# Performance work log

Measured on AMD Instinct MI355X. Metric: run time of the kernel, lower is better.

The kernel has to match this reference:

```python
import jax, jax.numpy as jnp
import numpy as np

B, NQ, S, D = 8, 1024, 2048, 512

def setup_inputs() -> dict:
    key = jax.random.key(0)
    k1, k2, k3, k4 = jax.random.split(key, 4)
    queries = jax.random.normal(k1, (B, NQ, D), dtype=jnp.float32)
    keys = jax.random.normal(k2, (B, S, D), dtype=jnp.float32)
    values = jax.random.normal(k3, (B, S, D), dtype=jnp.float32)
    mask = jax.random.randint(k4, (B, NQ, S), 0, 2, dtype=jnp.int32)
    return {"queries": queries, "keys": keys, "values": values, "mask": mask}

def reference(queries, keys, values, mask):
    # scores: dot-product attention scores (b, nq, s)
    scores = jnp.einsum('bqd,bsd->bqs', queries, keys)
    attention_dist = jax.nn.softmax(scores, axis=2)
    # mask then renormalize over seq axis
    attention_dist = attention_dist * mask.astype(attention_dist.dtype)
    attention_dist = attention_dist / attention_dist.sum(axis=2, keepdims=True)
    # weighted sum of values: equivalent to (dist.unsqueeze(3) * values.unsqueeze(1)).sum(2)
    final_vector = jnp.einsum('bqs,bsd->bqd', attention_dist, values)
    return final_vector
```

## Files before the change

kernel.cpp:

```cpp
#include <hip/hip_runtime.h>


#define Bz 8
#define NQz 1024
#define Sz 2048
#define Dz 512
#define QT 32
#define TS 32
#define NT ((Sz / 2) / TS)
#define KP 520
#define PP 40

typedef _Float16 f16x8 __attribute__((ext_vector_type(8)));
typedef float f32x4 __attribute__((ext_vector_type(4)));
typedef unsigned short ushort_t;

#define AS1(p) ((const __attribute__((address_space(1))) unsigned int*)(p))
#define AS3(p) ((__attribute__((address_space(3))) unsigned int*)(p))
#define DRAIN_ALL() __builtin_amdgcn_s_waitcnt(0)

__device__ __forceinline__ ushort_t f2h(float x) {
  _Float16 h = (_Float16)x;
  return __builtin_bit_cast(ushort_t, h);
}
__device__ __forceinline__ float h2f(ushort_t u) {
  return (float)__builtin_bit_cast(_Float16, u);
}

__global__ __launch_bounds__(256)
void prep(const float* __restrict__ K, const float* __restrict__ V,
          ushort_t* __restrict__ Kf, ushort_t* __restrict__ Vt) {
  __shared__ ushort_t sT[32][72];
  const int t = threadIdx.x;
  int bx = blockIdx.x;
  if (bx < 8192) {
    size_t e = ((size_t)bx * 256 + t) * 4;
    float4 v = *(const float4*)(K + e);
    uint2 w;
    w.x = (unsigned)f2h(v.x) | ((unsigned)f2h(v.y) << 16);
    w.y = (unsigned)f2h(v.z) | ((unsigned)f2h(v.w) << 16);
    *(uint2*)(Kf + e) = w;
    return;
  }
  bx -= 8192;
  const int b = bx >> 9;
  const int rest = bx & 511;
  const int st = rest >> 3;
  const int dt = rest & 7;
  const int s0 = st * 32, d0 = dt * 64;
  const float* Vb = V + ((size_t)b * Sz + s0) * Dz + d0;
#pragma unroll
  for (int i = 0; i < 2; ++i) {
    int idx = t + 256 * i;
    int s = idx >> 4;
    int dc = (idx & 15) * 4;
    float4 v = *(const float4*)(Vb + (size_t)s * Dz + dc);
    uint2 w;
    w.x = (unsigned)f2h(v.x) | ((unsigned)f2h(v.y) << 16);
    w.y = (unsigned)f2h(v.z) | ((unsigned)f2h(v.w) << 16);
    *(uint2*)(&sT[s][dc]) = w;
  }
  __syncthreads();
  ushort_t* VtB = Vt + ((size_t)b * Dz + d0) * Sz + s0;
  {
    int d = t >> 2, c = t & 3;
    uint4 u;
    ushort_t* tp = (ushort_t*)&u;
#pragma unroll
    for (int j = 0; j < 8; ++j) tp[j] = sT[c * 8 + j][d];
    *(uint4*)(VtB + (size_t)d * Sz + c * 8) = u;
  }
}

__global__ __launch_bounds__(256, 2)
void attn_flash(const float* __restrict__ Q, const int* __restrict__ Msk,
                const ushort_t* __restrict__ Kf, const ushort_t* __restrict__ Vt,
                float* __restrict__ Opart, float* __restrict__ Mpart,
                float* __restrict__ Lpart) {
  __shared__ ushort_t sK[TS][KP];
  __shared__ ushort_t sV[Dz][TS];
  __shared__ ushort_t sP[QT][PP];
  __shared__ float sTMax[2][QT];
  __shared__ float sTSum[2][QT];
  __shared__ float sM[2][QT];
  __shared__ float sL[2][QT];

  const int tid  = threadIdx.x;
  const int wave = tid >> 6;
  const int lane = tid & 63;
  const int l16  = lane & 15;
  const int quad = lane >> 4;
  const int rw   = wave & 1;
  const int cw   = wave >> 1;

  const int bx = blockIdx.x;
  const int b  = bx >> 6;
  const int r6 = bx & 63;
  const int qt = r6 >> 1;
  const int sh = r6 & 1;
  const int q0 = qt * QT;
  const int sbeg = sh * (Sz / 2);

  const float*    Qb  = Q  + ((size_t)b * NQz + q0) * Dz;
  const ushort_t* KfB = Kf + (size_t)b * Sz * Dz;
  const ushort_t* VtB = Vt + (size_t)b * Dz * Sz;
  const int*      Mb  = Msk + ((size_t)b * NQz + q0) * (size_t)Sz;

  int msk_r[4];

  auto issue_k = [&](int s0n) {
#pragma unroll
    for (int j = 0; j < 8; ++j) {
      int row = wave * 8 + j;
      const ushort_t* gp = KfB + (size_t)(s0n + row) * Dz + lane * 8;
      __builtin_amdgcn_global_load_lds(AS1(gp), AS3(&sK[row][0]), 16, 0, 0);
    }
  };
  auto issue_v = [&](int s0n) {
#pragma unroll
    for (int j = 0; j < 8; ++j) {
      int dbase = wave * 128 + j * 16;
      const ushort_t* gp =
          VtB + (size_t)(dbase + (lane >> 2)) * Sz + s0n + (lane & 3) * 8;
      __builtin_amdgcn_global_load_lds(AS1(gp), AS3(&sV[dbase][0]), 16, 0, 0);
    }
  };
  auto load_mask = [&](int s0n) {
    const int4 mv = *(const int4*)(Mb + (size_t)(rw * 16 + l16) * Sz + s0n +
                                   cw * 16 + quad * 4);
    msk_r[0] = mv.x; msk_r[1] = mv.y; msk_r[2] = mv.z; msk_r[3] = mv.w;
  };

  issue_k(sbeg);
  load_mask(sbeg);

  f16x8 qa[16];
  {
    const float* qrow = Qb + (size_t)(rw * 16 + l16) * Dz;
#pragma unroll
    for (int kk = 0; kk < 16; ++kk) {
      const float4 a = *(const float4*)(qrow + kk * 32 + quad * 8);
      const float4 c = *(const float4*)(qrow + kk * 32 + quad * 8 + 4);
      f16x8 h;
      h[0] = (_Float16)a.x; h[1] = (_Float16)a.y;
      h[2] = (_Float16)a.z; h[3] = (_Float16)a.w;
      h[4] = (_Float16)c.x; h[5] = (_Float16)c.y;
      h[6] = (_Float16)c.z; h[7] = (_Float16)c.w;
      qa[kk] = h;
    }
  }

  if (tid < QT) { sM[0][tid] = -1e30f; sL[0][tid] = 0.0f; }

  f32x4 oacc[16];
#pragma unroll
  for (int t = 0; t < 16; ++t) oacc[t] = (f32x4){0.f, 0.f, 0.f, 0.f};

  int p = 0;
  for (int i = 0; i < NT; ++i) {
    const int s0 = sbeg + i * TS;
    const int sNext = (i + 1 < NT) ? s0 + TS : sbeg;

    DRAIN_ALL();
    __syncthreads();

    issue_v(s0);

    f32x4 sc0 = (f32x4){0.f, 0.f, 0.f, 0.f};
    f32x4 sc1 = (f32x4){0.f, 0.f, 0.f, 0.f};
    {
      const ushort_t* kh = &sK[cw * 16 + l16][quad * 8];
#pragma unroll
      for (int kk = 0; kk < 16; kk += 2) {
        f16x8 b0 = *(const f16x8*)(kh + kk * 32);
        f16x8 b1 = *(const f16x8*)(kh + kk * 32 + 32);
        sc0 = __builtin_amdgcn_mfma_f32_16x16x32_f16(b0, qa[kk], sc0, 0, 0, 0);
        sc1 = __builtin_amdgcn_mfma_f32_16x16x32_f16(b1, qa[kk + 1], sc1, 0, 0, 0);
      }
    }
    f32x4 sc;
#pragma unroll
    for (int r = 0; r < 4; ++r) sc[r] = sc0[r] + sc1[r];

    float se[4];
#pragma unroll
    for (int r = 0; r < 4; ++r) se[r] = msk_r[r] ? sc[r] : -1e30f;
    float rmax = fmaxf(fmaxf(se[0], se[1]), fmaxf(se[2], se[3]));
    rmax = fmaxf(rmax, __shfl_xor(rmax, 16));
    rmax = fmaxf(rmax, __shfl_xor(rmax, 32));
    ushort_t pb[4];
    float rsum = 0.f;
#pragma unroll
    for (int r = 0; r < 4; ++r) {
      float pv = msk_r[r] ? __expf(se[r] - rmax) : 0.0f;
      pb[r] = f2h(pv);
      rsum += h2f(pb[r]);
    }
    {
      uint2 w;
      w.x = (unsigned)pb[0] | ((unsigned)pb[1] << 16);
      w.y = (unsigned)pb[2] | ((unsigned)pb[3] << 16);
      *(uint2*)(&sP[rw * 16 + l16][cw * 16 + quad * 4]) = w;
    }
    rsum += __shfl_xor(rsum, 16);
    rsum += __shfl_xor(rsum, 32);
    if (quad == 0) {
      sTMax[cw][rw * 16 + l16] = rmax;
      sTSum[cw][rw * 16 + l16] = rsum;
    }

    DRAIN_ALL();
    __syncthreads();

    issue_k(sNext);
    load_mask(sNext);

    const int pr = p;
    {
      const int row16 = rw * 16 + l16;
      float t0v = sTMax[0][row16], t1v = sTMax[1][row16];
      float mo16 = sM[pr][row16];
      float mn16 = fmaxf(mo16, fmaxf(t0v, t1v));
      float scl = __expf(((quad >> 1) ? t1v : t0v) - mn16);
      f16x8 praw = *(const f16x8*)(&sP[row16][quad * 8]);
      f16x8 pa;
#pragma unroll
      for (int j = 0; j < 8; ++j) pa[j] = (_Float16)((float)praw[j] * scl);

      float alpha[4];
#pragma unroll
      for (int r = 0; r < 4; ++r) {
        int rc = rw * 16 + quad * 4 + r;
        float a0 = sTMax[0][rc], a1 = sTMax[1][rc];
        float mo = sM[pr][rc];
        float mn = fmaxf(mo, fmaxf(a0, a1));
        float al = __expf(mo - mn);
        alpha[r] = al;
        if (cw == 0 && l16 == 0) {
          sM[pr ^ 1][rc] = mn;
          sL[pr ^ 1][rc] = al * sL[pr][rc] + __expf(a0 - mn) * sTSum[0][rc]
                                           + __expf(a1 - mn) * sTSum[1][rc];
        }
      }
#pragma unroll
      for (int t = 0; t < 16; ++t) {
#pragma unroll
        for (int r = 0; r < 4; ++r) oacc[t][r] *= alpha[r];
      }
#pragma unroll
      for (int t = 0; t < 16; ++t) {
        f16x8 vb = *(const f16x8*)(&sV[cw * 256 + t * 16 + l16][quad * 8]);
        oacc[t] = __builtin_amdgcn_mfma_f32_16x16x32_f16(pa, vb, oacc[t], 0, 0, 0);
      }
    }
    p ^= 1;
  }

  DRAIN_ALL();
  __syncthreads();
  const size_t rbase = (size_t)(b * 2 + sh) * NQz + q0;
#pragma unroll
  for (int t = 0; t < 16; ++t) {
#pragma unroll
    for (int r = 0; r < 4; ++r) {
      int rowq = rw * 16 + quad * 4 + r;
      Opart[(rbase + rowq) * Dz + cw * 256 + t * 16 + l16] = oacc[t][r];
    }
  }
  if (tid < QT) {
    Mpart[rbase + tid] = sM[p][tid];
    Lpart[rbase + tid] = sL[p][tid];
  }
}

__global__ __launch_bounds__(256)
void combine(const float* __restrict__ Opart, const float* __restrict__ Mpart,
             const float* __restrict__ Lpart, float* __restrict__ Out) {
  int gid = blockIdx.x * 256 + threadIdx.x;
  int row = gid >> 7;
  int b   = row >> 10;
  int q   = row & 1023;
  int c   = (gid & 127) * 4;
  size_t i0 = (size_t)(b * 2 + 0) * NQz + q;
  size_t i1 = (size_t)(b * 2 + 1) * NQz + q;
  float m0 = Mpart[i0], m1 = Mpart[i1];
  float l0 = Lpart[i0], l1 = Lpart[i1];
  float m  = fmaxf(m0, m1);
  float w0 = __expf(m0 - m), w1 = __expf(m1 - m);
  float inv = 1.0f / (w0 * l0 + w1 * l1);
  float4 a = *(const float4*)(Opart + i0 * Dz + c);
  float4 bv = *(const float4*)(Opart + i1 * Dz + c);
  float4 o;
  o.x = (w0 * a.x + w1 * bv.x) * inv;
  o.y = (w0 * a.y + w1 * bv.y) * inv;
  o.z = (w0 * a.z + w1 * bv.z) * inv;
  o.w = (w0 * a.w + w1 * bv.w) * inv;
  *(float4*)(Out + ((size_t)b * NQz + q) * Dz + c) = o;
}

extern "C" void kernel_launch(void* const* d_in, const int* in_sizes, int n_in,
                              void* d_out, int out_size, void* d_ws, size_t ws_size,
                              hipStream_t stream) {
  const float* Q = (const float*)d_in[0];
  const float* K = (const float*)d_in[1];
  const float* V = (const float*)d_in[2];
  const int*   M = (const int*)d_in[3];
  float* O = (float*)d_out;

  const size_t NKV = (size_t)Bz * Sz * Dz;
  ushort_t* Kf = (ushort_t*)d_ws;
  ushort_t* Vt = Kf + NKV;
  float* Opart = (float*)(Vt + NKV);
  float* Mpart = Opart + (size_t)Bz * 2 * NQz * Dz;
  float* Lpart = Mpart + (size_t)Bz * 2 * NQz;

  prep<<<dim3(12288), dim3(256), 0, stream>>>(K, V, Kf, Vt);
  attn_flash<<<dim3(512), dim3(256), 0, stream>>>(Q, M, Kf, Vt, Opart, Mpart, Lpart);
  combine<<<dim3(4096), dim3(256), 0, stream>>>(Opart, Mpart, Lpart, O);
}
```

Baseline: 257.0 us.

## Double-buffer K tiles, read V from global into registers, repartition PV work

```diff
diff --git a/kernel.cpp b/kernel.cpp
--- a/kernel.cpp
+++ b/kernel.cpp
@@ -30,7 +30,7 @@
 __global__ __launch_bounds__(256)
 void prep(const float* __restrict__ K, const float* __restrict__ V,
           ushort_t* __restrict__ Kf, ushort_t* __restrict__ Vt) {
-  __shared__ ushort_t sT[32][72];
+  __shared__ ushort_t sT[64][41];
   const int t = threadIdx.x;
   int bx = blockIdx.x;
   if (bx < 8192) {
@@ -45,15 +45,15 @@
   bx -= 8192;
   const int b = bx >> 9;
   const int rest = bx & 511;
-  const int st = rest >> 3;
-  const int dt = rest & 7;
-  const int s0 = st * 32, d0 = dt * 64;
+  const int st = rest >> 4;
+  const int dt = rest & 15;
+  const int s0 = st * 64, d0 = dt * 32;
   const float* Vb = V + ((size_t)b * Sz + s0) * Dz + d0;
 #pragma unroll
   for (int i = 0; i < 2; ++i) {
     int idx = t + 256 * i;
-    int s = idx >> 4;
-    int dc = (idx & 15) * 4;
+    int s = idx >> 3;
+    int dc = (idx & 7) * 4;
     float4 v = *(const float4*)(Vb + (size_t)s * Dz + dc);
     uint2 w;
     w.x = (unsigned)f2h(v.x) | ((unsigned)f2h(v.y) << 16);
@@ -63,7 +63,7 @@
   __syncthreads();
   ushort_t* VtB = Vt + ((size_t)b * Dz + d0) * Sz + s0;
   {
-    int d = t >> 2, c = t & 3;
+    int d = t >> 3, c = t & 7;
     uint4 u;
     ushort_t* tp = (ushort_t*)&u;
 #pragma unroll
@@ -77,8 +77,7 @@
                 const ushort_t* __restrict__ Kf, const ushort_t* __restrict__ Vt,
                 float* __restrict__ Opart, float* __restrict__ Mpart,
                 float* __restrict__ Lpart) {
-  __shared__ ushort_t sK[TS][KP];
-  __shared__ ushort_t sV[Dz][TS];
+  __shared__ ushort_t sK[2][TS][KP];
   __shared__ ushort_t sP[QT][PP];
   __shared__ float sTMax[2][QT];
   __shared__ float sTSum[2][QT];
@@ -93,7 +92,8 @@
   const int rw   = wave & 1;
   const int cw   = wave >> 1;
 
-  const int bx = blockIdx.x;
+  int bxr = blockIdx.x;
+  const int bx = (bxr & 7) * 64 + (bxr >> 3);
   const int b  = bx >> 6;
   const int r6 = bx & 63;
   const int qt = r6 >> 1;
@@ -106,33 +106,21 @@
   const ushort_t* VtB = Vt + (size_t)b * Dz * Sz;
   const int*      Mb  = Msk + ((size_t)b * NQz + q0) * (size_t)Sz;
 
-  int msk_r[4];
-
-  auto issue_k = [&](int s0n) {
+  auto issue_k = [&](int s0n, int bsel) {
 #pragma unroll
     for (int j = 0; j < 8; ++j) {
       int row = wave * 8 + j;
       const ushort_t* gp = KfB + (size_t)(s0n + row) * Dz + lane * 8;
-      __builtin_amdgcn_global_load_lds(AS1(gp), AS3(&sK[row][0]), 16, 0, 0);
+      __builtin_amdgcn_global_load_lds(AS1(gp), AS3(&sK[bsel][row][0]), 16, 0, 0);
     }
   };
-  auto issue_v = [&](int s0n) {
-#pragma unroll
-    for (int j = 0; j < 8; ++j) {
-      int dbase = wave * 128 + j * 16;
-      const ushort_t* gp =
-          VtB + (size_t)(dbase + (lane >> 2)) * Sz + s0n + (lane & 3) * 8;
-      __builtin_amdgcn_global_load_lds(AS1(gp), AS3(&sV[dbase][0]), 16, 0, 0);
-    }
+  auto load_mask = [&](int s0n) -> int4 {
+    return *(const int4*)(Mb + (size_t)(rw * 16 + l16) * Sz + s0n +
+                          cw * 16 + quad * 4);
   };
-  auto load_mask = [&](int s0n) {
-    const int4 mv = *(const int4*)(Mb + (size_t)(rw * 16 + l16) * Sz + s0n +
-                                   cw * 16 + quad * 4);
-    msk_r[0] = mv.x; msk_r[1] = mv.y; msk_r[2] = mv.z; msk_r[3] = mv.w;
-  };
-
-  issue_k(sbeg);
-  load_mask(sbeg);
+
+  issue_k(sbeg, 0);
+  int4 msk_cur = load_mask(sbeg);
 
   f16x8 qa[16];
   {
@@ -159,17 +147,21 @@
   int p = 0;
   for (int i = 0; i < NT; ++i) {
     const int s0 = sbeg + i * TS;
-    const int sNext = (i + 1 < NT) ? s0 + TS : sbeg;
+    const int bsel = i & 1;
 
     DRAIN_ALL();
     __syncthreads();
 
-    issue_v(s0);
+    int4 msk_nxt{0, 0, 0, 0};
+    if (i + 1 < NT) {
+      issue_k(s0 + TS, bsel ^ 1);
+      msk_nxt = load_mask(s0 + TS);
+    }
 
     f32x4 sc0 = (f32x4){0.f, 0.f, 0.f, 0.f};
     f32x4 sc1 = (f32x4){0.f, 0.f, 0.f, 0.f};
     {
-      const ushort_t* kh = &sK[cw * 16 + l16][quad * 8];
+      const ushort_t* kh = &sK[bsel][cw * 16 + l16][quad * 8];
 #pragma unroll
       for (int kk = 0; kk < 16; kk += 2) {
         f16x8 b0 = *(const f16x8*)(kh + kk * 32);
@@ -182,6 +174,7 @@
 #pragma unroll
     for (int r = 0; r < 4; ++r) sc[r] = sc0[r] + sc1[r];
 
+    int msk_r[4] = {msk_cur.x, msk_cur.y, msk_cur.z, msk_cur.w};
     float se[4];
 #pragma unroll
     for (int r = 0; r < 4; ++r) se[r] = msk_r[r] ? sc[r] : -1e30f;
@@ -209,50 +202,74 @@
       sTSum[cw][rw * 16 + l16] = rsum;
     }
 
-    DRAIN_ALL();
-    __syncthreads();
-
-    issue_k(sNext);
-    load_mask(sNext);
+    f16x8 vb[8];
+#pragma unroll
+    for (int dt = 0; dt < 8; ++dt) {
+      vb[dt] = *(const f16x8*)(VtB +
+          (size_t)(wave * 128 + dt * 16 + l16) * Sz + s0 + quad * 8);
+    }
+
+    asm volatile("s_waitcnt lgkmcnt(0)" ::: "memory");
+    __builtin_amdgcn_s_barrier();
+    asm volatile("" ::: "memory");
 
     const int pr = p;
-    {
-      const int row16 = rw * 16 + l16;
+    f16x8 pa[2];
+#pragma unroll
+    for (int rt = 0; rt < 2; ++rt) {
+      const int row16 = rt * 16 + l16;
       float t0v = sTMax[0][row16], t1v = sTMax[1][row16];
       float mo16 = sM[pr][row16];
       float mn16 = fmaxf(mo16, fmaxf(t0v, t1v));
       float scl = __expf(((quad >> 1) ? t1v : t0v) - mn16);
       f16x8 praw = *(const f16x8*)(&sP[row16][quad * 8]);
-      f16x8 pa;
-#pragma unroll
-      for (int j = 0; j < 8; ++j) pa[j] = (_Float16)((float)praw[j] * scl);
-
-      float alpha[4];
+      _Float16 sh16 = (_Float16)scl;
+#pragma unroll
+      for (int j = 0; j < 8; ++j) pa[rt][j] = praw[j] * sh16;
+    }
+
+    float dd[2][4];
+    bool grow = false;
+#pragma unroll
+    for (int rt = 0; rt < 2; ++rt) {
 #pragma unroll
       for (int r = 0; r < 4; ++r) {
-        int rc = rw * 16 + quad * 4 + r;
+        const int rc = rt * 16 + quad * 4 + r;
         float a0 = sTMax[0][rc], a1 = sTMax[1][rc];
         float mo = sM[pr][rc];
         float mn = fmaxf(mo, fmaxf(a0, a1));
-        float al = __expf(mo - mn);
-        alpha[r] = al;
-        if (cw == 0 && l16 == 0) {
+        dd[rt][r] = mo - mn;
+        grow = grow || (mn > mo);
+        if (wave == 0 && l16 == 0) {
           sM[pr ^ 1][rc] = mn;
-          sL[pr ^ 1][rc] = al * sL[pr][rc] + __expf(a0 - mn) * sTSum[0][rc]
-                                           + __expf(a1 - mn) * sTSum[1][rc];
+          sL[pr ^ 1][rc] = __expf(mo - mn) * sL[pr][rc]
+                         + __expf(a0 - mn) * sTSum[0][rc]
+                         + __expf(a1 - mn) * sTSum[1][rc];
         }
       }
-#pragma unroll
-      for (int t = 0; t < 16; ++t) {
-#pragma unroll
-        for (int r = 0; r < 4; ++r) oacc[t][r] *= alpha[r];
+    }
+    if (__any((int)grow)) {
+      float al[2][4];
+#pragma unroll
+      for (int rt = 0; rt < 2; ++rt)
+#pragma unroll
+        for (int r = 0; r < 4; ++r) al[rt][r] = __expf(dd[rt][r]);
+#pragma unroll
+      for (int t = 0; t < 16; ++t)
+#pragma unroll
+        for (int r = 0; r < 4; ++r) oacc[t][r] *= al[t >> 3][r];
+    }
+
+#pragma unroll
+    for (int dt = 0; dt < 8; ++dt) {
+#pragma unroll
+      for (int rt = 0; rt < 2; ++rt) {
+        oacc[rt * 8 + dt] = __builtin_amdgcn_mfma_f32_16x16x32_f16(
+            pa[rt], vb[dt], oacc[rt * 8 + dt], 0, 0, 0);
       }
-#pragma unroll
-      for (int t = 0; t < 16; ++t) {
-        f16x8 vb = *(const f16x8*)(&sV[cw * 256 + t * 16 + l16][quad * 8]);
-        oacc[t] = __builtin_amdgcn_mfma_f32_16x16x32_f16(pa, vb, oacc[t], 0, 0, 0);
-      }
-    }
+    }
+
+    msk_cur = msk_nxt;
     p ^= 1;
   }
 
@@ -263,8 +280,8 @@
   for (int t = 0; t < 16; ++t) {
 #pragma unroll
     for (int r = 0; r < 4; ++r) {
-      int rowq = rw * 16 + quad * 4 + r;
-      Opart[(rbase + rowq) * Dz + cw * 256 + t * 16 + l16] = oacc[t][r];
+      int rowq = (t >> 3) * 16 + quad * 4 + r;
+      Opart[(rbase + rowq) * Dz + wave * 128 + (t & 7) * 16 + l16] = oacc[t][r];
     }
   }
   if (tid < QT) {
```

Result: slower. 285.9 us (+11.3%).

## Pack mask to bits in prep, remap blocks, skip redundant O rescaling

Applied to the files above, without the earlier changes.

```diff
diff --git a/kernel.cpp b/kernel.cpp
--- a/kernel.cpp
+++ b/kernel.cpp
@@ -29,8 +29,9 @@
 
 __global__ __launch_bounds__(256)
 void prep(const float* __restrict__ K, const float* __restrict__ V,
-          ushort_t* __restrict__ Kf, ushort_t* __restrict__ Vt) {
-  __shared__ ushort_t sT[32][72];
+          const int* __restrict__ Mi, ushort_t* __restrict__ Kf,
+          ushort_t* __restrict__ Vt, unsigned* __restrict__ Mp) {
+  __shared__ ushort_t sT[64][41];
   const int t = threadIdx.x;
   int bx = blockIdx.x;
   if (bx < 8192) {
@@ -43,37 +44,49 @@
     return;
   }
   bx -= 8192;
-  const int b = bx >> 9;
-  const int rest = bx & 511;
-  const int st = rest >> 3;
-  const int dt = rest & 7;
-  const int s0 = st * 32, d0 = dt * 64;
-  const float* Vb = V + ((size_t)b * Sz + s0) * Dz + d0;
-#pragma unroll
-  for (int i = 0; i < 2; ++i) {
-    int idx = t + 256 * i;
-    int s = idx >> 4;
-    int dc = (idx & 15) * 4;
-    float4 v = *(const float4*)(Vb + (size_t)s * Dz + dc);
-    uint2 w;
-    w.x = (unsigned)f2h(v.x) | ((unsigned)f2h(v.y) << 16);
-    w.y = (unsigned)f2h(v.z) | ((unsigned)f2h(v.w) << 16);
-    *(uint2*)(&sT[s][dc]) = w;
-  }
-  __syncthreads();
-  ushort_t* VtB = Vt + ((size_t)b * Dz + d0) * Sz + s0;
-  {
-    int d = t >> 2, c = t & 3;
+  if (bx < 4096) {
+    const int b = bx >> 9;
+    const int rest = bx & 511;
+    const int st = rest >> 4;
+    const int dt = rest & 15;
+    const int s0 = st * 64, d0 = dt * 32;
+    const float* Vb = V + ((size_t)b * Sz + s0) * Dz + d0;
+#pragma unroll
+    for (int i = 0; i < 2; ++i) {
+      int idx = t + 256 * i;
+      int s = idx >> 3;
+      int dc = (idx & 7) * 4;
+      float4 v = *(const float4*)(Vb + (size_t)s * Dz + dc);
+      uint2 w;
+      w.x = (unsigned)f2h(v.x) | ((unsigned)f2h(v.y) << 16);
+      w.y = (unsigned)f2h(v.z) | ((unsigned)f2h(v.w) << 16);
+      *(uint2*)(&sT[s][dc]) = w;
+    }
+    __syncthreads();
+    ushort_t* VtB = Vt + ((size_t)b * Dz + d0) * Sz + s0;
+    int d = t >> 3, c = t & 7;
     uint4 u;
     ushort_t* tp = (ushort_t*)&u;
 #pragma unroll
     for (int j = 0; j < 8; ++j) tp[j] = sT[c * 8 + j][d];
     *(uint4*)(VtB + (size_t)d * Sz + c * 8) = u;
-  }
+    return;
+  }
+  bx -= 4096;
+  const int lane = t & 63;
+  const size_t base = (size_t)bx * 1024 + t * 4;
+  const int4 mv = *(const int4*)(Mi + base);
+  unsigned nib = (mv.x ? 1u : 0u) | (mv.y ? 2u : 0u) |
+                 (mv.z ? 4u : 0u) | (mv.w ? 8u : 0u);
+  unsigned v = nib << ((lane & 7) * 4);
+  v |= __shfl_xor(v, 1);
+  v |= __shfl_xor(v, 2);
+  v |= __shfl_xor(v, 4);
+  if ((lane & 7) == 0) Mp[bx * 32 + (t >> 3)] = v;
 }
 
 __global__ __launch_bounds__(256, 2)
-void attn_flash(const float* __restrict__ Q, const int* __restrict__ Msk,
+void attn_flash(const float* __restrict__ Q, const unsigned* __restrict__ Mp,
                 const ushort_t* __restrict__ Kf, const ushort_t* __restrict__ Vt,
                 float* __restrict__ Opart, float* __restrict__ Mpart,
                 float* __restrict__ Lpart) {
@@ -93,7 +106,8 @@
   const int rw   = wave & 1;
   const int cw   = wave >> 1;
 
-  const int bx = blockIdx.x;
+  int bxr = blockIdx.x;
+  const int bx = (bxr & 7) * 64 + (bxr >> 3);
   const int b  = bx >> 6;
   const int r6 = bx & 63;
   const int qt = r6 >> 1;
@@ -104,9 +118,7 @@
   const float*    Qb  = Q  + ((size_t)b * NQz + q0) * Dz;
   const ushort_t* KfB = Kf + (size_t)b * Sz * Dz;
   const ushort_t* VtB = Vt + (size_t)b * Dz * Sz;
-  const int*      Mb  = Msk + ((size_t)b * NQz + q0) * (size_t)Sz;
-
-  int msk_r[4];
+  const unsigned* MpB = Mp + ((size_t)b * NQz + q0) * (Sz / 32);
 
   auto issue_k = [&](int s0n) {
 #pragma unroll
@@ -125,14 +137,12 @@
       __builtin_amdgcn_global_load_lds(AS1(gp), AS3(&sV[dbase][0]), 16, 0, 0);
     }
   };
-  auto load_mask = [&](int s0n) {
-    const int4 mv = *(const int4*)(Mb + (size_t)(rw * 16 + l16) * Sz + s0n +
-                                   cw * 16 + quad * 4);
-    msk_r[0] = mv.x; msk_r[1] = mv.y; msk_r[2] = mv.z; msk_r[3] = mv.w;
+  auto load_mask = [&](int s0n) -> unsigned {
+    return MpB[(size_t)(rw * 16 + l16) * (Sz / 32) + (s0n >> 5)];
   };
 
   issue_k(sbeg);
-  load_mask(sbeg);
+  unsigned msk_cur = load_mask(sbeg);
 
   f16x8 qa[16];
   {
@@ -182,9 +192,10 @@
 #pragma unroll
     for (int r = 0; r < 4; ++r) sc[r] = sc0[r] + sc1[r];
 
+    const unsigned mbits = msk_cur >> (cw * 16 + quad * 4);
     float se[4];
 #pragma unroll
-    for (int r = 0; r < 4; ++r) se[r] = msk_r[r] ? sc[r] : -1e30f;
+    for (int r = 0; r < 4; ++r) se[r] = ((mbits >> r) & 1u) ? sc[r] : -1e30f;
     float rmax = fmaxf(fmaxf(se[0], se[1]), fmaxf(se[2], se[3]));
     rmax = fmaxf(rmax, __shfl_xor(rmax, 16));
     rmax = fmaxf(rmax, __shfl_xor(rmax, 32));
@@ -192,7 +203,7 @@
     float rsum = 0.f;
 #pragma unroll
     for (int r = 0; r < 4; ++r) {
-      float pv = msk_r[r] ? __expf(se[r] - rmax) : 0.0f;
+      float pv = ((mbits >> r) & 1u) ? __expf(se[r] - rmax) : 0.0f;
       pb[r] = f2h(pv);
       rsum += h2f(pb[r]);
     }
@@ -213,9 +224,10 @@
     __syncthreads();
 
     issue_k(sNext);
-    load_mask(sNext);
+    unsigned msk_nxt = load_mask(sNext);
 
     const int pr = p;
+    f16x8 pa;
     {
       const int row16 = rw * 16 + l16;
       float t0v = sTMax[0][row16], t1v = sTMax[1][row16];
@@ -223,36 +235,45 @@
       float mn16 = fmaxf(mo16, fmaxf(t0v, t1v));
       float scl = __expf(((quad >> 1) ? t1v : t0v) - mn16);
       f16x8 praw = *(const f16x8*)(&sP[row16][quad * 8]);
-      f16x8 pa;
-#pragma unroll
-      for (int j = 0; j < 8; ++j) pa[j] = (_Float16)((float)praw[j] * scl);
-
-      float alpha[4];
-#pragma unroll
-      for (int r = 0; r < 4; ++r) {
-        int rc = rw * 16 + quad * 4 + r;
-        float a0 = sTMax[0][rc], a1 = sTMax[1][rc];
-        float mo = sM[pr][rc];
-        float mn = fmaxf(mo, fmaxf(a0, a1));
-        float al = __expf(mo - mn);
-        alpha[r] = al;
-        if (cw == 0 && l16 == 0) {
-          sM[pr ^ 1][rc] = mn;
-          sL[pr ^ 1][rc] = al * sL[pr][rc] + __expf(a0 - mn) * sTSum[0][rc]
-                                           + __expf(a1 - mn) * sTSum[1][rc];
-        }
+      _Float16 sh16 = (_Float16)scl;
+#pragma unroll
+      for (int j = 0; j < 8; ++j) pa[j] = praw[j] * sh16;
+    }
+
+    float dd[4];
+    bool grow = false;
+#pragma unroll
+    for (int r = 0; r < 4; ++r) {
+      const int rc = rw * 16 + quad * 4 + r;
+      float a0 = sTMax[0][rc], a1 = sTMax[1][rc];
+      float mo = sM[pr][rc];
+      float mn = fmaxf(mo, fmaxf(a0, a1));
+      dd[r] = mo - mn;
+      grow = grow || (mn > mo);
+      if (cw == 0 && l16 == 0) {
+        sM[pr ^ 1][rc] = mn;
+        sL[pr ^ 1][rc] = __expf(mo - mn) * sL[pr][rc]
+                       + __expf(a0 - mn) * sTSum[0][rc]
+                       + __expf(a1 - mn) * sTSum[1][rc];
       }
-#pragma unroll
-      for (int t = 0; t < 16; ++t) {
-#pragma unroll
-        for (int r = 0; r < 4; ++r) oacc[t][r] *= alpha[r];
-      }
-#pragma unroll
-      for (int t = 0; t < 16; ++t) {
-        f16x8 vb = *(const f16x8*)(&sV[cw * 256 + t * 16 + l16][quad * 8]);
-        oacc[t] = __builtin_amdgcn_mfma_f32_16x16x32_f16(pa, vb, oacc[t], 0, 0, 0);
-      }
-    }
+    }
+    if (__any((int)grow)) {
+      float al[4];
+#pragma unroll
+      for (int r = 0; r < 4; ++r) al[r] = __expf(dd[r]);
+#pragma unroll
+      for (int t = 0; t < 16; ++t)
+#pragma unroll
+        for (int r = 0; r < 4; ++r) oacc[t][r] *= al[r];
+    }
+
+#pragma unroll
+    for (int t = 0; t < 16; ++t) {
+      f16x8 vb = *(const f16x8*)(&sV[cw * 256 + t * 16 + l16][quad * 8]);
+      oacc[t] = __builtin_amdgcn_mfma_f32_16x16x32_f16(pa, vb, oacc[t], 0, 0, 0);
+    }
+
+    msk_cur = msk_nxt;
     p ^= 1;
   }
 
@@ -313,8 +334,9 @@
   float* Opart = (float*)(Vt + NKV);
   float* Mpart = Opart + (size_t)Bz * 2 * NQz * Dz;
   float* Lpart = Mpart + (size_t)Bz * 2 * NQz;
-
-  prep<<<dim3(12288), dim3(256), 0, stream>>>(K, V, Kf, Vt);
-  attn_flash<<<dim3(512), dim3(256), 0, stream>>>(Q, M, Kf, Vt, Opart, Mpart, Lpart);
+  unsigned* Mp = (unsigned*)(Lpart + (size_t)Bz * 2 * NQz);
+
+  prep<<<dim3(28672), dim3(256), 0, stream>>>(K, V, M, Kf, Vt, Mp);
+  attn_flash<<<dim3(512), dim3(256), 0, stream>>>(Q, Mp, Kf, Vt, Opart, Mpart, Lpart);
   combine<<<dim3(4096), dim3(256), 0, stream>>>(Opart, Mpart, Lpart, O);
 }
```

New measurement: 265.5 us. 1.03x slower.
